# Performance work log

Measured on AMD Instinct MI355X. Metric: run time of the kernel, lower is better.

Reference implementation:

```python
import math
import jax, jax.numpy as jnp
import numpy as np

# ---- config (mirrors ModelConfig) ----
B, T = 2, 2048
N_EMBD, N_HEAD, N_KV = 2048, 16, 4
DH = N_EMBD // N_HEAD          # 128
G = N_HEAD // N_KV             # 4
ROPE_THETA = 1e6
YARN_FACTOR = 64.0
ORIG_MAX_POS = 4096
BETA_FAST, BETA_SLOW = 4.0, 1.0
MSCALE, MSCALE_ALL_DIM = 1.0, 0.0


def _yarn_get_mscale(scale, mscale=1.0):
    if scale <= 1.0:
        return 1.0
    return 0.1 * mscale * math.log(scale) + 1.0


def yarn_inv_freq_and_factor():
    dim = DH
    base = ROPE_THETA
    factor = YARN_FACTOR
    if MSCALE and MSCALE_ALL_DIM:
        attn_factor = _yarn_get_mscale(factor, MSCALE) / _yarn_get_mscale(factor, MSCALE_ALL_DIM)
    else:
        attn_factor = _yarn_get_mscale(factor)

    def corr_dim(num_rot):
        return dim * math.log(ORIG_MAX_POS / (num_rot * 2 * math.pi)) / (2 * math.log(base))

    low = max(math.floor(corr_dim(BETA_FAST)), 0.0)
    high = min(math.ceil(corr_dim(BETA_SLOW)), float(dim - 1))
    if low == high:
        high += 0.001
    half = dim // 2
    t = np.arange(half, dtype=np.float32)
    ramp = np.clip((t - low) / (high - low), 0.0, 1.0)  # linear ramp
    pos = np.arange(0, dim, 2, dtype=np.float32) / dim
    pos_freqs = base ** pos
    inv_extrap = 1.0 / pos_freqs
    inv_interp = 1.0 / (factor * pos_freqs)
    extrap_factor = 1.0 - ramp
    inv = inv_interp * (1.0 - extrap_factor) + inv_extrap * extrap_factor
    return jnp.asarray(inv, jnp.float32), float(attn_factor)


INV_FREQ, ATTN_FACTOR = yarn_inv_freq_and_factor()


def apply_rope_yarn(x, positions, inv_freq, attn_factor):
    # x: [B, T, H, Dh] interleaved RoPE, then scale by attn_factor
    x32 = x.astype(jnp.float32)
    angles = positions.astype(jnp.float32)[:, None] * inv_freq[None, :]  # [T, Dh/2]
    cos = angles[None, :, None, :]  # broadcast shapes
    cos, sin = jnp.cos(cos), jnp.sin(angles)[None, :, None, :]
    x_even = x32[..., 0::2]
    x_odd = x32[..., 1::2]
    out_even = x_even * cos - x_odd * sin
    out_odd = x_even * sin + x_odd * cos
    out = jnp.stack([out_even, out_odd], axis=-1).reshape(x.shape)
    return (out * attn_factor).astype(x.dtype)


def setup_inputs() -> dict:
    key = jax.random.key(0)
    k1, k2, k3 = jax.random.split(key, 3)
    x = jax.random.normal(k1, (B, T, N_EMBD), jnp.float32)
    w_qkv = jax.random.normal(k2, (N_EMBD, N_EMBD + 2 * N_KV * DH), jnp.float32) * (N_EMBD ** -0.5)
    w_o = jax.random.normal(k3, (N_EMBD, N_EMBD), jnp.float32) * (N_EMBD ** -0.5)
    return {"x": x, "w_qkv": w_qkv, "w_o": w_o}


def reference(x, w_qkv, w_o):
    qkv = x @ w_qkv  # [B, T, n_embd + 2*n_kv*dh]
    q_raw = qkv[:, :, :N_EMBD]
    k_raw = qkv[:, :, N_EMBD:N_EMBD + N_KV * DH]
    v_raw = qkv[:, :, N_EMBD + N_KV * DH:]
    q = q_raw.reshape(B, T, N_HEAD, DH)
    k = k_raw.reshape(B, T, N_KV, DH)
    v = v_raw.reshape(B, T, N_KV, DH)

    pos = jnp.arange(T, dtype=jnp.int32)
    q = apply_rope_yarn(q, pos, INV_FREQ, ATTN_FACTOR)
    k = apply_rope_yarn(k, pos, INV_FREQ, ATTN_FACTOR)

    q = q.reshape(B, T, N_KV, G, DH).transpose(0, 2, 3, 1, 4)  # [B, kv, g, T, Dh]
    k = k.transpose(0, 2, 1, 3)  # [B, kv, T, Dh]
    v = v.transpose(0, 2, 1, 3)  # [B, kv, T, Dh]

    scale = 1.0 / math.sqrt(DH)
    att = jnp.einsum('bkgtd,bksd->bkgts', q, k) * scale
    causal = jnp.tril(jnp.ones((T, T), bool))[None, None, None]
    att = jnp.where(causal, att, jnp.asarray(-1e9, att.dtype))
    w = jax.nn.softmax(att, axis=-1)
    y = jnp.einsum('bkgts,bksd->bkgtd', w, v)
    y = y.transpose(0, 3, 1, 2, 4).reshape(B, T, N_EMBD)
    return y @ w_o
```

## Files before the change

### kernel.cpp

```cpp
#include <hip/hip_runtime.h>
#include <hip/hip_bf16.h>
#include <math.h>

#define B_    2
#define T_    2048
#define CEMB  2048
#define NH    16
#define NKV   4
#define DHD   128
#define QKVD  3072

typedef unsigned short u16;
typedef unsigned int   u32;
typedef __attribute__((ext_vector_type(8))) short  short8;
typedef __attribute__((ext_vector_type(4))) float  floatx4;

static __device__ __forceinline__ u16 f2bf(float f){
    union{float f;u32 u;}x; x.f = f; u32 u = x.u;
    return (u16)((u + 0x7fffu + ((u >> 16) & 1u)) >> 16);
}
static __device__ __forceinline__ float lo2f(u32 w){ union{u32 u;float f;}x; x.u = w << 16; return x.f; }
static __device__ __forceinline__ float hi2f(u32 w){ union{u32 u;float f;}x; x.u = w & 0xffff0000u; return x.f; }

static __device__ __forceinline__ u32 cvt_pk_bf16(float lo, float hi){
    u32 r;
    asm("v_cvt_pk_bf16_f32 %0, %1, %2" : "=v"(r) : "v"(lo), "v"(hi));
    return r;
}

static __device__ __forceinline__ void async_cp16(const u16* g, u16* lds_wave_base) {
    __builtin_amdgcn_global_load_lds(
        (const __attribute__((address_space(1))) void*)g,
        (__attribute__((address_space(3))) void*)lds_wave_base, 16, 0, 0);
}

__global__ __launch_bounds__(256) void convert_kernel(const float* __restrict__ in,
                                                      u16* __restrict__ out, int n8)
{
    const int i = blockIdx.x * 256 + threadIdx.x;
    if (i >= n8) return;
    const float4* p = reinterpret_cast<const float4*>(in);
    float4 a = p[i * 2], b = p[i * 2 + 1];
    uint4 o;
    o.x = (u32)f2bf(a.x) | ((u32)f2bf(a.y) << 16);
    o.y = (u32)f2bf(a.z) | ((u32)f2bf(a.w) << 16);
    o.z = (u32)f2bf(b.x) | ((u32)f2bf(b.y) << 16);
    o.w = (u32)f2bf(b.z) | ((u32)f2bf(b.w) << 16);
    reinterpret_cast<uint4*>(out)[i] = o;
}

__global__ __launch_bounds__(256) void transpose_f32_bf16(const float* __restrict__ in,
                                                          u16* __restrict__ out,
                                                          int R, int Cn)
{
    __shared__ float tl[32][33];
    const int tx = threadIdx.x & 31, ty = threadIdx.x >> 5;
    const int c0 = blockIdx.x << 5, r0 = blockIdx.y << 5;
    #pragma unroll
    for (int i = 0; i < 4; ++i)
        tl[ty + i * 8][tx] = in[(size_t)(r0 + ty + i * 8) * Cn + c0 + tx];
    __syncthreads();
    #pragma unroll
    for (int i = 0; i < 4; ++i)
        out[(size_t)(c0 + ty + i * 8) * R + r0 + tx] = f2bf(tl[tx][ty + i * 8]);
}

__global__ __launch_bounds__(256) void vt_build_kernel(const u16* __restrict__ qkv,
                                                       u16* __restrict__ vt)
{
    __shared__ u16 tl[32][33];
    const int tx = threadIdx.x & 31, ty = threadIdx.x >> 5;
    const int t0 = blockIdx.x << 5, d0 = blockIdx.y << 5;
    const int b = blockIdx.z >> 2, kv = blockIdx.z & 3;
    #pragma unroll
    for (int i = 0; i < 4; ++i)
        tl[ty + i * 8][tx] =
            qkv[(size_t)(b * T_ + t0 + ty + i * 8) * QKVD + CEMB + NKV * DHD + kv * DHD + d0 + tx];
    __syncthreads();
    #pragma unroll
    for (int i = 0; i < 4; ++i)
        vt[(size_t)((b * NKV + kv) * DHD + d0 + ty + i * 8) * T_ + t0 + tx] = tl[tx][ty + i * 8];
}

template <bool F32OUT>
__global__ __launch_bounds__(256) void gemm_mfma_kernel(const u16* __restrict__ A,
                                                        const u16* __restrict__ BT,
                                                        void* __restrict__ Cv,
                                                        int M, int N, int K)
{
    __shared__ u16 As[128 * 32];
    __shared__ u16 Bs[128 * 32];
    const int tid  = threadIdx.x;
    const int lane = tid & 63;
    const int wv   = tid >> 6;
    const int n16  = lane & 15;
    const int quad = lane >> 4;
    const int wm   = wv >> 1, wn = wv & 1;
    const int row0 = blockIdx.y << 7;
    const int col0 = blockIdx.x << 7;

    floatx4 acc[4][4];
    #pragma unroll
    for (int i = 0; i < 4; ++i)
        #pragma unroll
        for (int j = 0; j < 4; ++j) acc[i][j] = (floatx4)0.0f;

    for (int k0 = 0; k0 < K; k0 += 32) {
        __syncthreads();
        #pragma unroll
        for (int it = 0; it < 2; ++it) {
            const int idx = it * 256 + tid;
            const int m = idx >> 2, k8 = (idx & 3) << 3;
            async_cp16(A  + (size_t)(row0 + m) * K + k0 + k8, &As[(it * 256 + wv * 64) * 8]);
            async_cp16(BT + (size_t)(col0 + m) * K + k0 + k8, &Bs[(it * 256 + wv * 64) * 8]);
        }
        __syncthreads();
        short8 af[4], bf[4];
        #pragma unroll
        for (int mt = 0; mt < 4; ++mt)
            af[mt] = *reinterpret_cast<const short8*>(&As[(wm * 64 + mt * 16 + n16) * 32 + quad * 8]);
        #pragma unroll
        for (int nt = 0; nt < 4; ++nt)
            bf[nt] = *reinterpret_cast<const short8*>(&Bs[(wn * 64 + nt * 16 + n16) * 32 + quad * 8]);
        #pragma unroll
        for (int mt = 0; mt < 4; ++mt)
            #pragma unroll
            for (int nt = 0; nt < 4; ++nt)
                acc[mt][nt] = __builtin_amdgcn_mfma_f32_16x16x32_bf16(af[mt], bf[nt], acc[mt][nt], 0, 0, 0);
    }
    #pragma unroll
    for (int mt = 0; mt < 4; ++mt) {
        #pragma unroll
        for (int r = 0; r < 4; ++r) {
            const int row = row0 + wm * 64 + mt * 16 + quad * 4 + r;
            if (F32OUT) {
                float* C = reinterpret_cast<float*>(Cv);
                #pragma unroll
                for (int nt = 0; nt < 4; ++nt)
                    C[(size_t)row * N + col0 + wn * 64 + nt * 16 + n16] = acc[mt][nt][r];
            } else {
                u16* C = reinterpret_cast<u16*>(Cv);
                #pragma unroll
                for (int nt = 0; nt < 4; ++nt)
                    C[(size_t)row * N + col0 + wn * 64 + nt * 16 + n16] = f2bf(acc[mt][nt][r]);
            }
        }
    }
}

__global__ __launch_bounds__(256) void rope_kernel(
    u16* __restrict__ qkv, const float attn_factor, const float low, const float high)
{
    const int total = B_ * T_ * (NH + NKV) * (DHD / 2);
    int idx = blockIdx.x * 256 + threadIdx.x;
    if (idx >= total) return;
    const int d = idx & 63;
    int r = idx >> 6;
    const int h = r % (NH + NKV);
    r /= (NH + NKV);
    const int t = r % T_;
    const int b = r / T_;
    const int off = (h < NH) ? (h * DHD) : (CEMB + (h - NH) * DHD);

    u32* p = reinterpret_cast<u32*>(qkv + (size_t)(b * T_ + t) * QKVD + off) + d;
    u32 w = *p;
    float xe = lo2f(w), xo = hi2f(w);

    float df   = (float)d;
    float ramp = (df - low) / (high - low);
    ramp = fminf(fmaxf(ramp, 0.0f), 1.0f);
    float pf     = expf((2.0f * df / 128.0f) * 13.815510557964274f);
    float inv_ex = 1.0f / pf;
    float inv    = inv_ex * ((1.0f / 64.0f) * ramp + (1.0f - ramp));
    float ang = (float)t * inv;
    float s = sinf(ang), c = cosf(ang);
    float oe = (xe * c - xo * s) * attn_factor;
    float oo = (xe * s + xo * c) * attn_factor;
    *p = (u32)f2bf(oe) | ((u32)f2bf(oo) << 16);
}

__global__ __launch_bounds__(512, 4) void attn_mfma_kernel(const u16* __restrict__ qkv,
                                                           const u16* __restrict__ vt,
                                                           u16* __restrict__ y)
{
    __shared__ __align__(16) u16 Ksd[2][64 * 128];
    __shared__ __align__(16) u16 Vtsd[2][128 * 64];
    __shared__ __align__(16) u16 Pl[8 * 1024];

    const int tid  = threadIdx.x;
    const int lane = tid & 63;
    const int wv   = tid >> 6;
    const int n16  = lane & 15;
    const int quad = lane >> 4;

    const int lin = blockIdx.y * 16 + blockIdx.x;
    const int swz = (lin & 7) * 64 + (lin >> 3);
    const int nx  = swz & 15;
    const int bh  = swz >> 4;
    const int b   = bh >> 4;
    const int h   = bh & 15;
    const int kh  = h >> 2;

    const float C1 = 0.08838834764831845f * 1.4426950408889634f;

    u16* plw = Pl + wv * 1024;
    const int psw = (n16 & 7) << 3;

    const u16* kbase = qkv + (size_t)(b * T_) * QKVD + CEMB + kh * DHD;
    const u16* vbase = vt + (size_t)((b * NKV + kh) * DHD) * T_;

    auto dma_k = [&](int j0, int buf) {
        #pragma unroll
        for (int it = 0; it < 2; ++it) {
            const int P   = it * 512 + tid;
            const int row = P >> 4;
            const int lc  = (P & 15) ^ (row & 15);
            async_cp16(kbase + (size_t)(j0 + row) * QKVD + (lc << 3),
                       &Ksd[buf][(it * 512 + wv * 64) * 8]);
        }
    };
    auto dma_v = [&](int j0, int buf) {
        #pragma unroll
        for (int it = 0; it < 2; ++it) {
            const int P   = it * 512 + tid;
            const int row = P >> 3;
            const int lc  = (P & 7) ^ (row & 7);
            async_cp16(vbase + (size_t)row * T_ + j0 + (lc << 3),
                       &Vtsd[buf][(it * 512 + wv * 64) * 8]);
        }
    };

    const int i0H = (31 - nx) << 6;
    const int i0  = (wv < 4) ? i0H : (nx << 6);
    const int qb  = i0 + (wv & 3) * 16;
    const int qrow = qb + n16;

    const u16* qp = qkv + (size_t)(b * T_ + qrow) * QKVD + h * DHD;
    short8 qf[4];
    #pragma unroll
    for (int kk = 0; kk < 4; ++kk)
        qf[kk] = *reinterpret_cast<const short8*>(qp + kk * 32 + quad * 8);

    floatx4 oacc[8];
    #pragma unroll
    for (int i = 0; i < 8; ++i) oacc[i] = (floatx4)0.0f;
    float m_cur = -INFINITY, l_cur = 0.0f;

    dma_k(0, 0);
    dma_v(0, 0);

    for (int j0 = 0; j0 <= i0H; j0 += 64) {
        const int buf = (j0 >> 6) & 1;
        __syncthreads();
        if (j0 + 64 <= i0H) {
            dma_k(j0 + 64, buf ^ 1);
            dma_v(j0 + 64, buf ^ 1);
        }
        if (j0 > i0) continue;

        const u16* kb = Ksd[buf];
        const u16* vb = Vtsd[buf];

        floatx4 st[4];
        #pragma unroll
        for (int t = 0; t < 4; ++t) st[t] = (floatx4)0.0f;
        __builtin_amdgcn_s_setprio(1);
        #pragma unroll
        for (int t = 0; t < 4; ++t) {
            #pragma unroll
            for (int kk = 0; kk < 4; ++kk) {
                short8 a = *reinterpret_cast<const short8*>(
                    &kb[(t * 16 + n16) * 128 + (((kk * 4 + quad) ^ n16) << 3)]);
                st[t] = __builtin_amdgcn_mfma_f32_16x16x32_bf16(a, qf[kk], st[t], 0, 0, 0);
            }
        }
        __builtin_amdgcn_s_setprio(0);

        const bool diag = (j0 + 63 > qb);
        float tmax = -INFINITY;
        #pragma unroll
        for (int t = 0; t < 4; ++t) {
            if (diag) {
                #pragma unroll
                for (int r = 0; r < 4; ++r) {
                    const int key = j0 + t * 16 + quad * 4 + r;
                    if (key > qrow) st[t][r] = -INFINITY;
                }
            }
            tmax = fmaxf(tmax,
                         fmaxf(fmaxf(st[t][0], st[t][1]), fmaxf(st[t][2], st[t][3])));
        }
        tmax = fmaxf(tmax, __shfl_xor(tmax, 16));
        tmax = fmaxf(tmax, __shfl_xor(tmax, 32));

        if (!__all((tmax - m_cur) * C1 <= 8.0f)) {
            const float mnew  = fmaxf(m_cur, tmax);
            const float alpha = exp2f((m_cur - mnew) * C1);
            m_cur = mnew;
            l_cur *= alpha;
            #pragma unroll
            for (int dt = 0; dt < 8; ++dt) {
                oacc[dt][0] *= alpha; oacc[dt][1] *= alpha;
                oacc[dt][2] *= alpha; oacc[dt][3] *= alpha;
            }
        }

        const float mC = m_cur * C1;
        float lsum = 0.0f;
        #pragma unroll
        for (int t = 0; t < 4; ++t) {
            float p0 = exp2f(fmaf(st[t][0], C1, -mC));
            float p1 = exp2f(fmaf(st[t][1], C1, -mC));
            float p2 = exp2f(fmaf(st[t][2], C1, -mC));
            float p3 = exp2f(fmaf(st[t][3], C1, -mC));
            lsum += (p0 + p1) + (p2 + p3);
            uint2 pk;
            pk.x = cvt_pk_bf16(p0, p1);
            pk.y = cvt_pk_bf16(p2, p3);
            *reinterpret_cast<uint2*>(&plw[n16 * 64 + ((t * 16 + quad * 4) ^ psw)]) = pk;
        }
        lsum += __shfl_xor(lsum, 16);
        lsum += __shfl_xor(lsum, 32);
        l_cur += lsum;

        __builtin_amdgcn_s_setprio(1);
        #pragma unroll
        for (int kt = 0; kt < 2; ++kt) {
            short8 pfrag = *reinterpret_cast<const short8*>(
                &plw[n16 * 64 + ((kt * 32 + quad * 8) ^ psw)]);
            #pragma unroll
            for (int dt = 0; dt < 8; ++dt) {
                short8 vfrag = *reinterpret_cast<const short8*>(
                    &vb[(dt * 16 + n16) * 64 + (((kt * 4 + quad) ^ (n16 & 7)) << 3)]);
                oacc[dt] = __builtin_amdgcn_mfma_f32_16x16x32_bf16(vfrag, pfrag, oacc[dt], 0, 0, 0);
            }
        }
        __builtin_amdgcn_s_setprio(0);
    }

    const float linv = 1.0f / l_cur;
    u16* yp = y + (size_t)(b * T_ + qrow) * CEMB + h * DHD + quad * 4;
    #pragma unroll
    for (int dt = 0; dt < 8; ++dt) {
        float a0 = oacc[dt][0] * linv, a1 = oacc[dt][1] * linv;
        float a2 = oacc[dt][2] * linv, a3 = oacc[dt][3] * linv;
        u32 w0 = cvt_pk_bf16(a0, a1);
        u32 w1 = cvt_pk_bf16(a2, a3);
        *reinterpret_cast<u32*>(yp + dt * 16)     = w0;
        *reinterpret_cast<u32*>(yp + dt * 16 + 2) = w1;
    }
}

extern "C" void kernel_launch(void* const* d_in, const int* in_sizes, int n_in,
                              void* d_out, int out_size, void* d_ws, size_t ws_size,
                              hipStream_t stream) {
    const size_t NX   = (size_t)B_ * T_ * CEMB;
    const size_t NWQ  = (size_t)CEMB * QKVD;
    const size_t NWO  = (size_t)CEMB * CEMB;
    const size_t NQKV = (size_t)B_ * T_ * QKVD;
    const size_t NY   = NX;

    u16* qkv = (u16*)d_ws;
    u16* y   = qkv + NQKV;
    u16* xb  = y + NY;
    u16* wqT = xb + NX;
    u16* woT = wqT + NWQ;
    u16* vtb = xb;

    convert_kernel<<<(int)(NX / 8 + 255) / 256, 256, 0, stream>>>((const float*)d_in[0], xb, (int)(NX / 8));
    transpose_f32_bf16<<<dim3(QKVD / 32, CEMB / 32), 256, 0, stream>>>((const float*)d_in[1], wqT, CEMB, QKVD);
    transpose_f32_bf16<<<dim3(CEMB / 32, CEMB / 32), 256, 0, stream>>>((const float*)d_in[2], woT, CEMB, CEMB);

    gemm_mfma_kernel<false><<<dim3(QKVD / 128, (B_ * T_) / 128), 256, 0, stream>>>(
        xb, wqT, qkv, B_ * T_, QKVD, CEMB);

    const double two_pi = 6.283185307179586476925286766559;
    double corr4 = 128.0 * log(4096.0 / (4.0 * two_pi)) / (2.0 * log(1.0e6));
    double corr1 = 128.0 * log(4096.0 / (1.0 * two_pi)) / (2.0 * log(1.0e6));
    double lowd  = floor(corr4); if (lowd < 0.0) lowd = 0.0;
    double highd = ceil(corr1);  if (highd > 127.0) highd = 127.0;
    if (lowd == highd) highd += 0.001;
    float attn_factor = (float)(0.1 * log(64.0) + 1.0);

    const int rope_total = B_ * T_ * (NH + NKV) * (DHD / 2);
    rope_kernel<<<(rope_total + 255) / 256, 256, 0, stream>>>(
        qkv, attn_factor, (float)lowd, (float)highd);

    vt_build_kernel<<<dim3(T_ / 32, DHD / 32, B_ * NKV), 256, 0, stream>>>(qkv, vtb);

    attn_mfma_kernel<<<dim3(T_ / 128, B_ * NH), 512, 0, stream>>>(qkv, vtb, y);

    gemm_mfma_kernel<true><<<dim3(CEMB / 128, (B_ * T_) / 128), 256, 0, stream>>>(
        y, woT, d_out, B_ * T_, CEMB, CEMB);
}
```

Before: 320.9 us.

## Rewrite GEMMs with 512-thread blocks, double-buffered LDS, XOR swizzle and tile remap

Replaces the single-buffered 128x128x32 GEMM with a templated 256xBN, BK=64 kernel using 8 waves. It double-buffers global-to-LDS async copies with explicit vmcnt waits, XOR-swizzles LDS columns to avoid bank conflicts, remaps block indices for L2 locality, and raises wave priority around the MFMA bursts. The aim is to hide load latency and increase reuse per tile in both projection GEMMs. The cost is more LDS and registers per block, and with larger tiles fewer workgroups for the 4096-row problems.

```diff
diff --git a/kernel.cpp b/kernel.cpp
--- a/kernel.cpp
+++ b/kernel.cpp
@@ -82,67 +82,114 @@
         vt[(size_t)((b * NKV + kv) * DHD + d0 + ty + i * 8) * T_ + t0 + tx] = tl[tx][ty + i * 8];
 }
 
-template <bool F32OUT>
-__global__ __launch_bounds__(256) void gemm_mfma_kernel(const u16* __restrict__ A,
-                                                        const u16* __restrict__ BT,
-                                                        void* __restrict__ Cv,
-                                                        int M, int N, int K)
-{
-    __shared__ u16 As[128 * 32];
-    __shared__ u16 Bs[128 * 32];
+template <int BN_, int WM_, int WN_, bool F32OUT>
+__global__ __launch_bounds__(512, 2) void gemm_mfma8_kernel(const u16* __restrict__ A,
+                                                            const u16* __restrict__ BT,
+                                                            void* __restrict__ Cv,
+                                                            int M, int N, int K)
+{
+    constexpr int BM = 256, BK = 64;
+    constexpr int MR = BM / WM_ / 16;
+    constexpr int NR = BN_ / WN_ / 16;
+    constexpr int AR = (BM * BK * 2) / 8192;
+    constexpr int BR = (BN_ * BK * 2) / 8192;
+    constexpr int LPT = AR + BR;
+
+    __shared__ __align__(16) u16 As[2][BM * BK];
+    __shared__ __align__(16) u16 Bs[2][BN_ * BK];
+
     const int tid  = threadIdx.x;
     const int lane = tid & 63;
     const int wv   = tid >> 6;
     const int n16  = lane & 15;
     const int quad = lane >> 4;
-    const int wm   = wv >> 1, wn = wv & 1;
-    const int row0 = blockIdx.y << 7;
-    const int col0 = blockIdx.x << 7;
-
-    floatx4 acc[4][4];
-    #pragma unroll
-    for (int i = 0; i < 4; ++i)
-        #pragma unroll
-        for (int j = 0; j < 4; ++j) acc[i][j] = (floatx4)0.0f;
-
-    for (int k0 = 0; k0 < K; k0 += 32) {
-        __syncthreads();
-        #pragma unroll
-        for (int it = 0; it < 2; ++it) {
-            const int idx = it * 256 + tid;
-            const int m = idx >> 2, k8 = (idx & 3) << 3;
-            async_cp16(A  + (size_t)(row0 + m) * K + k0 + k8, &As[(it * 256 + wv * 64) * 8]);
-            async_cp16(BT + (size_t)(col0 + m) * K + k0 + k8, &Bs[(it * 256 + wv * 64) * 8]);
-        }
-        __syncthreads();
-        short8 af[4], bf[4];
-        #pragma unroll
-        for (int mt = 0; mt < 4; ++mt)
-            af[mt] = *reinterpret_cast<const short8*>(&As[(wm * 64 + mt * 16 + n16) * 32 + quad * 8]);
-        #pragma unroll
-        for (int nt = 0; nt < 4; ++nt)
-            bf[nt] = *reinterpret_cast<const short8*>(&Bs[(wn * 64 + nt * 16 + n16) * 32 + quad * 8]);
-        #pragma unroll
-        for (int mt = 0; mt < 4; ++mt)
-            #pragma unroll
-            for (int nt = 0; nt < 4; ++nt)
-                acc[mt][nt] = __builtin_amdgcn_mfma_f32_16x16x32_bf16(af[mt], bf[nt], acc[mt][nt], 0, 0, 0);
+    const int wm   = wv / WN_;
+    const int wn   = wv % WN_;
+
+    const int GX  = gridDim.x;
+    const int nwg = GX * gridDim.y;
+    const int lin = blockIdx.y * GX + blockIdx.x;
+    const int swz = (lin & 7) * (nwg >> 3) + (lin >> 3);
+    const int row0 = (swz / GX) * BM;
+    const int col0 = (swz % GX) * BN_;
+
+    auto stage = [&](int t, int buf) {
+        const int k0 = t * BK;
+        const int rA = tid >> 3;
+        const int lc = (tid & 7) ^ (rA & 7);
+        #pragma unroll
+        for (int r = 0; r < AR; ++r)
+            async_cp16(A + (size_t)(row0 + r * 64 + rA) * K + k0 + (lc << 3),
+                       &As[buf][(r * 512 + wv * 64) * 8]);
+        #pragma unroll
+        for (int r = 0; r < BR; ++r)
+            async_cp16(BT + (size_t)(col0 + r * 64 + rA) * K + k0 + (lc << 3),
+                       &Bs[buf][(r * 512 + wv * 64) * 8]);
+    };
+
+    floatx4 acc[MR][NR];
+    #pragma unroll
+    for (int m = 0; m < MR; ++m)
+        #pragma unroll
+        for (int n = 0; n < NR; ++n) acc[m][n] = (floatx4)0.0f;
+
+    const int nt = K / BK;
+    stage(0, 0);
+    stage(1, 1);
+
+    for (int t = 0; t < nt; ++t) {
+        const int cur = t & 1;
+        if (t + 1 < nt) asm volatile("s_waitcnt vmcnt(%0)" :: "i"(LPT) : "memory");
+        else            asm volatile("s_waitcnt vmcnt(0)" ::: "memory");
+        __builtin_amdgcn_s_barrier();
+
+        const u16* as = As[cur];
+        const u16* bs = Bs[cur];
+        #pragma unroll
+        for (int kh = 0; kh < 2; ++kh) {
+            short8 af[MR], bf[NR];
+            #pragma unroll
+            for (int m = 0; m < MR; ++m) {
+                const int row = wm * (BM / WM_) + m * 16 + n16;
+                af[m] = *reinterpret_cast<const short8*>(
+                    &as[row * BK + (((kh * 4 + quad) ^ (row & 7)) << 3)]);
+            }
+            #pragma unroll
+            for (int n = 0; n < NR; ++n) {
+                const int col = wn * (BN_ / WN_) + n * 16 + n16;
+                bf[n] = *reinterpret_cast<const short8*>(
+                    &bs[col * BK + (((kh * 4 + quad) ^ (col & 7)) << 3)]);
+            }
+            __builtin_amdgcn_s_setprio(1);
+            #pragma unroll
+            for (int m = 0; m < MR; ++m)
+                #pragma unroll
+                for (int n = 0; n < NR; ++n)
+                    acc[m][n] = __builtin_amdgcn_mfma_f32_16x16x32_bf16(af[m], bf[n], acc[m][n], 0, 0, 0);
+            __builtin_amdgcn_s_setprio(0);
+        }
+
+        asm volatile("s_waitcnt lgkmcnt(0)" ::: "memory");
+        __builtin_amdgcn_s_barrier();
+        __builtin_amdgcn_sched_barrier(0);
+        if (t + 2 < nt) stage(t + 2, cur);
     }
-    #pragma unroll
-    for (int mt = 0; mt < 4; ++mt) {
+
+    #pragma unroll
+    for (int m = 0; m < MR; ++m) {
         #pragma unroll
         for (int r = 0; r < 4; ++r) {
-            const int row = row0 + wm * 64 + mt * 16 + quad * 4 + r;
+            const int row = row0 + wm * (BM / WM_) + m * 16 + quad * 4 + r;
             if (F32OUT) {
                 float* C = reinterpret_cast<float*>(Cv);
                 #pragma unroll
-                for (int nt = 0; nt < 4; ++nt)
-                    C[(size_t)row * N + col0 + wn * 64 + nt * 16 + n16] = acc[mt][nt][r];
+                for (int n = 0; n < NR; ++n)
+                    C[(size_t)row * N + col0 + wn * (BN_ / WN_) + n * 16 + n16] = acc[m][n][r];
             } else {
                 u16* C = reinterpret_cast<u16*>(Cv);
                 #pragma unroll
-                for (int nt = 0; nt < 4; ++nt)
-                    C[(size_t)row * N + col0 + wn * 64 + nt * 16 + n16] = f2bf(acc[mt][nt][r]);
+                for (int n = 0; n < NR; ++n)
+                    C[(size_t)row * N + col0 + wn * (BN_ / WN_) + n * 16 + n16] = f2bf(acc[m][n][r]);
             }
         }
     }
@@ -371,7 +418,7 @@
     transpose_f32_bf16<<<dim3(QKVD / 32, CEMB / 32), 256, 0, stream>>>((const float*)d_in[1], wqT, CEMB, QKVD);
     transpose_f32_bf16<<<dim3(CEMB / 32, CEMB / 32), 256, 0, stream>>>((const float*)d_in[2], woT, CEMB, CEMB);
 
-    gemm_mfma_kernel<false><<<dim3(QKVD / 128, (B_ * T_) / 128), 256, 0, stream>>>(
+    gemm_mfma8_kernel<192, 2, 4, false><<<dim3(QKVD / 192, (B_ * T_) / 256), 512, 0, stream>>>(
         xb, wqT, qkv, B_ * T_, QKVD, CEMB);
 
     const double two_pi = 6.283185307179586476925286766559;
@@ -390,6 +437,6 @@
 
     attn_mfma_kernel<<<dim3(T_ / 128, B_ * NH), 512, 0, stream>>>(qkv, vtb, y);
 
-    gemm_mfma_kernel<true><<<dim3(CEMB / 128, (B_ * T_) / 128), 256, 0, stream>>>(
+    gemm_mfma8_kernel<128, 4, 2, true><<<dim3(CEMB / 128, (B_ * T_) / 256), 512, 0, stream>>>(
         y, woT, d_out, B_ * T_, CEMB, CEMB);
 }
```

After: 299.3 us. -6.7%, faster.
